# Kernel tuning notes

Measured on AMD Instinct MI355X. Metric: run time of the kernel, lower is better.

Reference implementation:

```python
import jax, jax.numpy as jnp
import numpy as np

COMMITMENT_COST = 0.25

def _l2norm(v, axis=-1, eps=1e-12):
    # matches F.normalize(p=2): v / max(||v||, eps)
    n = jnp.sqrt(jnp.sum(v * v, axis=axis, keepdims=True))
    return v / jnp.maximum(n, eps)

def setup_inputs() -> dict:
    key = jax.random.key(0)
    k1, k2 = jax.random.split(key)
    N, D, K = 131072, 64, 2048
    x = jax.random.normal(k1, (N, D), dtype=jnp.float32)
    embeddings = jax.random.normal(k2, (K, D), dtype=jnp.float32)
    return {"x": x, "embeddings": embeddings}

def reference(x, embeddings):
    # x: [N, D] latents; embeddings: [K, D] codebook
    xn = _l2norm(x, axis=-1)                 # [N, D]
    en = _l2norm(embeddings, axis=-1)        # [K, D]
    # squared euclidean distances: ||xn||^2 + ||en||^2 - 2 xn.en
    d = (jnp.sum(xn * xn, axis=-1, keepdims=True)
         + jnp.sum(en * en, axis=-1)[None, :]
         - 2.0 * jnp.einsum('nd,kd->nk', xn, en))   # [N, K]
    idx = jnp.argmin(d, axis=1)              # [N] int
    quantized = en[idx]                      # [N, D] (already unit-norm; re-normalizing is idempotent but matches quantize())
    quantized = _l2norm(quantized, axis=-1)
    q_latent_loss = jnp.mean((quantized - jax.lax.stop_gradient(xn)) ** 2)
    e_latent_loss = jnp.mean((xn - jax.lax.stop_gradient(quantized)) ** 2)
    loss = q_latent_loss + COMMITMENT_COST * e_latent_loss
    # straight-through estimator
    quantized_st = xn + jax.lax.stop_gradient(quantized - xn)
    return quantized_st, loss, idx
```

## Files before the change

### kernel.cpp

```cpp
#include <hip/hip_runtime.h>
#include <math.h>
#include <stdint.h>


#define D 64
#define EPS 1e-12f
#define WPB 4
#define RG 2
#define RPW (RG * 16)
#define RPB (WPB * RPW)
#define CAP 832
#define MARGIN 0.010f

typedef short bf16x8 __attribute__((ext_vector_type(8)));
typedef float f32x4 __attribute__((ext_vector_type(4)));

__device__ __forceinline__ uint32_t f2bf(float f) {
    uint32_t u = __builtin_bit_cast(uint32_t, f);
    return (u + 0x7FFFu + ((u >> 16) & 1u)) >> 16;
}
__device__ __forceinline__ int xsw(int row, int d) {
    return row * 64 + ((((d >> 2) ^ (row & 7)) << 2) | (d & 3));
}

__global__ __launch_bounds__(1024) void vq_prep(const float* __restrict__ emb,
                                                float* __restrict__ en,
                                                float* __restrict__ en2,
                                                uint32_t* __restrict__ frags,
                                                float* __restrict__ loss_out,
                                                int K) {
    __shared__ float sh[16][64];
    int w = (int)(threadIdx.x >> 6), lane = (int)(threadIdx.x & 63);
    int tile = (int)blockIdx.x;
    int row = tile * 16 + w;
    if (row < K) {
        float v = emb[(size_t)row * D + lane];
        float s = v * v;
        #pragma unroll
        for (int m = 32; m >= 1; m >>= 1) s += __shfl_xor(s, m, 64);
        float e = v / fmaxf(sqrtf(s), EPS);
        float s2 = e * e;
        #pragma unroll
        for (int m = 32; m >= 1; m >>= 1) s2 += __shfl_xor(s2, m, 64);
        en[(size_t)row * D + lane] = e;
        if (lane == 0) en2[row] = s2;
        sh[w][lane] = e;
    }
    if (blockIdx.x == 0 && threadIdx.x == 0) loss_out[0] = 0.f;
    __syncthreads();
    if (w == 0) {
        int cl = lane & 15, dbase = (lane >> 4) * 8;
        #pragma unroll
        for (int h = 0; h < 2; ++h) {
            const float* p = &sh[cl][h * 32 + dbase];
            uint4 u;
            u.x = f2bf(p[0]) | (f2bf(p[1]) << 16);
            u.y = f2bf(p[2]) | (f2bf(p[3]) << 16);
            u.z = f2bf(p[4]) | (f2bf(p[5]) << 16);
            u.w = f2bf(p[6]) | (f2bf(p[7]) << 16);
            *(uint4*)(frags + ((size_t)(tile * 2 + h) * 64 + lane) * 4) = u;
        }
    }
}

__global__ __launch_bounds__(256, 4) void vq_main(const float* __restrict__ x,
                                                  const float* __restrict__ en,
                                                  const float* __restrict__ en2g,
                                                  const uint32_t* __restrict__ frags,
                                                  float* __restrict__ out_q,
                                                  float* __restrict__ out_idx,
                                                  float* __restrict__ loss_out,
                                                  int N, int K) {
    __shared__ float xn[RPB * 64];
    __shared__ uint16_t cand[WPB][CAP];
    __shared__ int candcnt[WPB];
    __shared__ unsigned long long keys[RPB];
    __shared__ double red[WPB];

    const int tid = (int)threadIdx.x;
    const int w = tid >> 6, lane = tid & 63;
    const int rowbase = (int)blockIdx.x * RPB;
    const int NT = K / 16;
    const int lq = (lane >> 4) << 2;

    for (int r = 0; r < RPW; ++r) {
        int rb = w * RPW + r;
        float v = x[(size_t)(rowbase + rb) * D + lane];
        float s = v * v;
        #pragma unroll
        for (int m = 32; m >= 1; m >>= 1) s += __shfl_xor(s, m, 64);
        xn[xsw(rb, lane)] = v / fmaxf(sqrtf(s), EPS);
    }
    if (lane == 0) candcnt[w] = 0;
    if (lane < RPW) keys[w * RPW + lane] = ~0ull;

    bf16x8 bfr[RG][2];
    #pragma unroll
    for (int g = 0; g < RG; ++g)
        #pragma unroll
        for (int h = 0; h < 2; ++h) {
            int row = w * RPW + g * 16 + (lane & 15);
            int db = h * 32 + ((lane >> 4) * 8);
            union { uint32_t u[4]; bf16x8 v; } cvt;
            #pragma unroll
            for (int j = 0; j < 4; ++j)
                cvt.u[j] = f2bf(xn[xsw(row, db + 2 * j)]) |
                           (f2bf(xn[xsw(row, db + 2 * j + 1)]) << 16);
            bfr[g][h] = cvt.v;
        }

    const f32x4 zero4 = {0.f, 0.f, 0.f, 0.f};
    const bf16x8* fb = (const bf16x8*)frags + lane;

    f32x4 rmax[RG];
    #pragma unroll
    for (int g = 0; g < RG; ++g) rmax[g] = {-3.0e38f, -3.0e38f, -3.0e38f, -3.0e38f};
    {
        const bf16x8* p = fb;
        bf16x8 A0 = p[0], A1 = p[64];
        for (int t = 0; t < NT; t += 2) {
            bf16x8 B0 = p[128], B1 = p[192];
            #pragma unroll
            for (int g = 0; g < RG; ++g) {
                f32x4 acc = __builtin_amdgcn_mfma_f32_16x16x32_bf16(A0, bfr[g][0], zero4, 0, 0, 0);
                acc = __builtin_amdgcn_mfma_f32_16x16x32_bf16(A1, bfr[g][1], acc, 0, 0, 0);
                #pragma unroll
                for (int q = 0; q < 4; ++q) rmax[g][q] = fmaxf(rmax[g][q], acc[q]);
            }
            if (t + 2 < NT) { A0 = p[256]; A1 = p[320]; }
            #pragma unroll
            for (int g = 0; g < RG; ++g) {
                f32x4 acc = __builtin_amdgcn_mfma_f32_16x16x32_bf16(B0, bfr[g][0], zero4, 0, 0, 0);
                acc = __builtin_amdgcn_mfma_f32_16x16x32_bf16(B1, bfr[g][1], acc, 0, 0, 0);
                #pragma unroll
                for (int q = 0; q < 4; ++q) rmax[g][q] = fmaxf(rmax[g][q], acc[q]);
            }
            p += 256;
            if (((t + 1) & 15) == 15) __syncthreads();
        }
    }
    float tau[RG];
    #pragma unroll
    for (int g = 0; g < RG; ++g) {
        float m = fmaxf(fmaxf(rmax[g][0], rmax[g][1]), fmaxf(rmax[g][2], rmax[g][3]));
        m = fmaxf(m, __shfl_xor(m, 16, 64));
        m = fmaxf(m, __shfl_xor(m, 32, 64));
        tau[g] = m - MARGIN;
    }

    {
        const bf16x8* p = fb;
        bf16x8 A0 = p[0], A1 = p[64];
        for (int t = 0; t < NT; ++t) {
            bf16x8 nA0, nA1;
            if (t + 1 < NT) { nA0 = p[128]; nA1 = p[192]; }
            int cb = t * 16 + lq;
            #pragma unroll
            for (int g = 0; g < RG; ++g) {
                f32x4 acc = __builtin_amdgcn_mfma_f32_16x16x32_bf16(A0, bfr[g][0], zero4, 0, 0, 0);
                acc = __builtin_amdgcn_mfma_f32_16x16x32_bf16(A1, bfr[g][1], acc, 0, 0, 0);
                float m4 = fmaxf(fmaxf(acc[0], acc[1]), fmaxf(acc[2], acc[3]));
                if (__any(m4 >= tau[g])) {
                    int rloc = g * 16 + (lane & 15);
                    #pragma unroll
                    for (int q = 0; q < 4; ++q) {
                        if (acc[q] >= tau[g]) {
                            int k = cb + q;
                            int slot = atomicAdd(&candcnt[w], 1);
                            if (slot < CAP) {
                                cand[w][slot] = (uint16_t)((k << 5) | rloc);
                            } else {
                                const float* ev = en + (size_t)k * D;
                                float dot = 0.f;
                                #pragma unroll
                                for (int d0 = 0; d0 < D; ++d0)
                                    dot = fmaf(xn[xsw(w * RPW + rloc, d0)], ev[d0], dot);
                                float R = fmaf(-0.5f, en2g[k], dot);
                                uint32_t fbt = __builtin_bit_cast(uint32_t, -R);
                                uint32_t ord = (fbt & 0x80000000u) ? ~fbt : (fbt | 0x80000000u);
                                atomicMin(&keys[w * RPW + rloc],
                                          ((unsigned long long)ord << 32) | (uint32_t)k);
                            }
                        }
                    }
                }
            }
            A0 = nA0; A1 = nA1;
            p += 128;
            if ((t & 15) == 15) __syncthreads();
        }
    }

    int cnt = candcnt[w];
    cnt = cnt < CAP ? cnt : CAP;
    for (int base = 0; base < cnt; base += 64) {
        int i = base + lane;
        if (i < cnt) {
            uint32_t e = cand[w][i];
            int k = (int)(e >> 5), rloc = (int)(e & 31u);
            const float* ev = en + (size_t)k * D;
            float dot = 0.f;
            #pragma unroll
            for (int d0 = 0; d0 < D; ++d0)
                dot = fmaf(xn[xsw(w * RPW + rloc, d0)], ev[d0], dot);
            float R = fmaf(-0.5f, en2g[k], dot);
            uint32_t fbt = __builtin_bit_cast(uint32_t, -R);
            uint32_t ord = (fbt & 0x80000000u) ? ~fbt : (fbt | 0x80000000u);
            atomicMin(&keys[w * RPW + rloc],
                      ((unsigned long long)ord << 32) | (uint32_t)k);
        }
    }

    float ls = 0.f;
    for (int r = 0; r < RPW; ++r) {
        int rb = w * RPW + r;
        int k = (int)(keys[rb] & 0x7FFull);
        float rn = fmaxf(sqrtf(en2g[k]), EPS);
        float q = en[(size_t)k * D + lane] / rn;
        float a = xn[xsw(rb, lane)];
        float dx = q - a;
        ls = fmaf(dx, dx, ls);
        out_q[(size_t)(rowbase + rb) * D + lane] = a + dx;
    }
    if (lane < RPW) out_idx[rowbase + w * RPW + lane] =
        (float)(int)(keys[w * RPW + lane] & 0x7FFull);
    #pragma unroll
    for (int m = 32; m >= 1; m >>= 1) ls += __shfl_xor(ls, m, 64);
    if (lane == 0) red[w] = (double)ls;
    __syncthreads();
    if (tid == 0) {
        double s = 0.0;
        #pragma unroll
        for (int i = 0; i < WPB; ++i) s += red[i];
        atomicAdd(loss_out, (float)(s * (1.25 / ((double)N * (double)D))));
    }
}

extern "C" void kernel_launch(void* const* d_in, const int* in_sizes, int n_in,
                              void* d_out, int out_size, void* d_ws, size_t ws_size,
                              hipStream_t stream) {
    const float* x   = (const float*)d_in[0];
    const float* emb = (const float*)d_in[1];
    int N = in_sizes[0] / D;
    int K = in_sizes[1] / D;

    float* out      = (float*)d_out;
    float* out_q    = out;
    float* loss_out = out + (size_t)N * D;
    float* out_idx  = out + (size_t)N * D + 1;

    char* ws = (char*)d_ws;
    float*    en2   = (float*)(ws + 8192);
    float*    en    = (float*)(ws + 16384);
    uint32_t* frags = (uint32_t*)(ws + 540672);

    vq_prep<<<K / 16, 1024, 0, stream>>>(emb, en, en2, frags, loss_out, K);
    vq_main<<<N / RPB, 256, 0, stream>>>(x, en, en2, frags, out_q, out_idx,
                                         loss_out, N, K);
}
```

Before: 184.0 us.

## Use 2 waves per block with 4 row groups per wave for B-fragment reuse

Blocks drop from 4 waves of 32 rows to 2 waves of 64 rows each, so every codebook fragment loaded from global memory feeds twice as many MFMAs. The candidate encoding is widened to 32 bits to hold 6-bit row indices. Row loads in the normalize and output loops are batched four at a time to overlap latency, and the intra-loop barrier moves to every 4 tiles. More rows per wave means more registers and fewer waves per block, which may lower occupancy and latency hiding, and the extra barriers add sync cost.

```diff
diff --git a/kernel.cpp b/kernel.cpp
--- a/kernel.cpp
+++ b/kernel.cpp
@@ -5,8 +5,8 @@
 
 #define D 64
 #define EPS 1e-12f
-#define WPB 4
-#define RG 2
+#define WPB 2
+#define RG 4
 #define RPW (RG * 16)
 #define RPB (WPB * RPW)
 #define CAP 832
@@ -63,7 +63,7 @@
     }
 }
 
-__global__ __launch_bounds__(256, 4) void vq_main(const float* __restrict__ x,
+__global__ __launch_bounds__(128, 2) void vq_main(const float* __restrict__ x,
                                                   const float* __restrict__ en,
                                                   const float* __restrict__ en2g,
                                                   const uint32_t* __restrict__ frags,
@@ -72,7 +72,7 @@
                                                   float* __restrict__ loss_out,
                                                   int N, int K) {
     __shared__ float xn[RPB * 64];
-    __shared__ uint16_t cand[WPB][CAP];
+    __shared__ uint32_t cand[WPB][CAP];
     __shared__ int candcnt[WPB];
     __shared__ unsigned long long keys[RPB];
     __shared__ double red[WPB];
@@ -83,16 +83,21 @@
     const int NT = K / 16;
     const int lq = (lane >> 4) << 2;
 
-    for (int r = 0; r < RPW; ++r) {
-        int rb = w * RPW + r;
-        float v = x[(size_t)(rowbase + rb) * D + lane];
-        float s = v * v;
-        #pragma unroll
-        for (int m = 32; m >= 1; m >>= 1) s += __shfl_xor(s, m, 64);
-        xn[xsw(rb, lane)] = v / fmaxf(sqrtf(s), EPS);
+    for (int r0 = 0; r0 < RPW; r0 += 4) {
+        float v[4];
+        #pragma unroll
+        for (int j = 0; j < 4; ++j)
+            v[j] = x[(size_t)(rowbase + w * RPW + r0 + j) * D + lane];
+        #pragma unroll
+        for (int j = 0; j < 4; ++j) {
+            float s = v[j] * v[j];
+            #pragma unroll
+            for (int m = 32; m >= 1; m >>= 1) s += __shfl_xor(s, m, 64);
+            xn[xsw(w * RPW + r0 + j, lane)] = v[j] / fmaxf(sqrtf(s), EPS);
+        }
     }
     if (lane == 0) candcnt[w] = 0;
-    if (lane < RPW) keys[w * RPW + lane] = ~0ull;
+    keys[tid] = ~0ull;
 
     bf16x8 bfr[RG][2];
     #pragma unroll
@@ -136,7 +141,7 @@
                 for (int q = 0; q < 4; ++q) rmax[g][q] = fmaxf(rmax[g][q], acc[q]);
             }
             p += 256;
-            if (((t + 1) & 15) == 15) __syncthreads();
+            if ((t & 3) == 2) __syncthreads();
         }
     }
     float tau[RG];
@@ -168,7 +173,7 @@
                             int k = cb + q;
                             int slot = atomicAdd(&candcnt[w], 1);
                             if (slot < CAP) {
-                                cand[w][slot] = (uint16_t)((k << 5) | rloc);
+                                cand[w][slot] = ((uint32_t)k << 6) | (uint32_t)rloc;
                             } else {
                                 const float* ev = en + (size_t)k * D;
                                 float dot = 0.f;
@@ -187,7 +192,7 @@
             }
             A0 = nA0; A1 = nA1;
             p += 128;
-            if ((t & 15) == 15) __syncthreads();
+            if ((t & 3) == 3) __syncthreads();
         }
     }
 
@@ -197,7 +202,7 @@
         int i = base + lane;
         if (i < cnt) {
             uint32_t e = cand[w][i];
-            int k = (int)(e >> 5), rloc = (int)(e & 31u);
+            int k = (int)(e >> 6), rloc = (int)(e & 63u);
             const float* ev = en + (size_t)k * D;
             float dot = 0.f;
             #pragma unroll
@@ -212,26 +217,33 @@
     }
 
     float ls = 0.f;
-    for (int r = 0; r < RPW; ++r) {
-        int rb = w * RPW + r;
-        int k = (int)(keys[rb] & 0x7FFull);
-        float rn = fmaxf(sqrtf(en2g[k]), EPS);
-        float q = en[(size_t)k * D + lane] / rn;
-        float a = xn[xsw(rb, lane)];
-        float dx = q - a;
-        ls = fmaf(dx, dx, ls);
-        out_q[(size_t)(rowbase + rb) * D + lane] = a + dx;
-    }
-    if (lane < RPW) out_idx[rowbase + w * RPW + lane] =
+    for (int r0 = 0; r0 < RPW; r0 += 4) {
+        int kk[4];
+        float qv[4];
+        #pragma unroll
+        for (int j = 0; j < 4; ++j)
+            kk[j] = (int)(keys[w * RPW + r0 + j] & 0x7FFull);
+        #pragma unroll
+        for (int j = 0; j < 4; ++j)
+            qv[j] = en[(size_t)kk[j] * D + lane];
+        #pragma unroll
+        for (int j = 0; j < 4; ++j) {
+            float rn = fmaxf(sqrtf(en2g[kk[j]]), EPS);
+            float q = qv[j] / rn;
+            float a = xn[xsw(w * RPW + r0 + j, lane)];
+            float dx = q - a;
+            ls = fmaf(dx, dx, ls);
+            out_q[(size_t)(rowbase + w * RPW + r0 + j) * D + lane] = a + dx;
+        }
+    }
+    out_idx[rowbase + w * RPW + lane] =
         (float)(int)(keys[w * RPW + lane] & 0x7FFull);
     #pragma unroll
     for (int m = 32; m >= 1; m >>= 1) ls += __shfl_xor(ls, m, 64);
     if (lane == 0) red[w] = (double)ls;
     __syncthreads();
     if (tid == 0) {
-        double s = 0.0;
-        #pragma unroll
-        for (int i = 0; i < WPB; ++i) s += red[i];
+        double s = red[0] + red[1];
         atomicAdd(loss_out, (float)(s * (1.25 / ((double)N * (double)D))));
     }
 }
@@ -255,6 +267,6 @@
     uint32_t* frags = (uint32_t*)(ws + 540672);
 
     vq_prep<<<K / 16, 1024, 0, stream>>>(emb, en, en2, frags, loss_out, K);
-    vq_main<<<N / RPB, 256, 0, stream>>>(x, en, en2, frags, out_q, out_idx,
+    vq_main<<<N / RPB, 128, 0, stream>>>(x, en, en2, frags, out_q, out_idx,
                                          loss_out, N, K);
 }
```

After: 200.7 us. 9.1% more time.
